# Kernel optimization log

Hardware: AMD Instinct MI355X
Metric: run time of the kernel (lower is better)

Reference implementation:

```python
import jax, jax.numpy as jnp
import numpy as np

# per-head local window sizes (== init local_region_shape); all divide H=W=64 -> no boundary masks
REGIONS = (4, 4, 8, 8, 16, 16, 32, 32)


def setup_inputs() -> dict:
    key = jax.random.key(0)
    ks = jax.random.split(key, 4)
    B, H, W, C = 4, 64, 64, 512
    N = H * W
    std = 0.02  # trunc_normal_(std=0.02) in the torch init
    return {
        "x": jax.random.normal(ks[0], (B, N, C), jnp.float32),
        "Wq": jax.random.normal(ks[1], (C, C), jnp.float32) * std,
        "Wkv": jax.random.normal(ks[2], (C, 2 * C), jnp.float32) * std,
        "Wproj": jax.random.normal(ks[3], (C, C), jnp.float32) * std,
        "bproj": jnp.zeros((C,), jnp.float32),
        "H": 64,
        "W": 64,
    }


def _to_windows(xh, H, W, r):
    # (B, N, d) -> (B*Hr*Wr, r*r, d), windows in row-major order (matches F.unfold k=stride=r)
    B, N, d = xh.shape
    Hr, Wr = H // r, W // r
    x = xh.reshape(B, Hr, r, Wr, r, d).transpose(0, 1, 3, 2, 4, 5)
    return x.reshape(B * Hr * Wr, r * r, d)


def _from_windows(xw, B, H, W, r):
    # inverse of _to_windows (matches F.fold k=stride=r)
    d = xw.shape[-1]
    Hr, Wr = H // r, W // r
    x = xw.reshape(B, Hr, Wr, r, r, d).transpose(0, 1, 3, 2, 4, 5)
    return x.reshape(B, H * W, d)


def reference(x, Wq, Wkv, Wproj, bproj, H, W):
    B, N, C = x.shape
    nh = len(REGIONS)
    hd = C // nh
    scale = hd ** -0.5
    q = (x @ Wq).reshape(B, N, nh, hd).transpose(0, 2, 1, 3)            # (B, nh, N, hd)
    kv = (x @ Wkv).reshape(B, N, 2, nh, hd).transpose(2, 0, 3, 1, 4)    # (2, B, nh, N, hd)
    k, v = kv[0], kv[1]
    outs = []
    for i, r in enumerate(REGIONS):
        qh, kh, vh = q[:, i], k[:, i], v[:, i]                          # (B, N, hd)
        if r == 1:
            attn = jax.nn.softmax(jnp.einsum("bqd,bkd->bqk", qh, kh) * scale, axis=-1)
            outs.append(jnp.einsum("bqk,bkd->bqd", attn, vh))
        else:
            qw = _to_windows(qh, H, W, r)                               # (B*nw, r*r, hd)
            kw = _to_windows(kh, H, W, r)
            vw = _to_windows(vh, H, W, r)
            attn = jax.nn.softmax(jnp.einsum("wqd,wkd->wqk", qw, kw) * scale, axis=-1)
            ow = jnp.einsum("wqk,wkd->wqd", attn, vw)
            outs.append(_from_windows(ow, B, H, W, r))
    o = jnp.stack(outs, axis=2).reshape(B, N, C)                        # heads interleaved per token
    return o @ Wproj + bproj
```

## Files before the change

kernel.cpp:

```cpp
#include <hip/hip_runtime.h>

typedef __attribute__((ext_vector_type(4))) float f32x4;
typedef __attribute__((ext_vector_type(8))) short s16x8;
typedef __attribute__((ext_vector_type(4))) unsigned int u32x4;
typedef __attribute__((ext_vector_type(2))) unsigned int u32x2;

#define LOG2E 1.44269504088896340736f

#define GLOAD_LDS16(g, l)                                                     \
    __builtin_amdgcn_global_load_lds((const __attribute__((address_space(1))) void*)(g), \
                                     (__attribute__((address_space(3))) void*)(l), 16, 0, 0)

__device__ inline unsigned short bf16_rne(float f) {
    unsigned u = __builtin_bit_cast(unsigned, f);
    unsigned r = u + 0x7FFFu + ((u >> 16) & 1u);
    return (unsigned short)(r >> 16);
}

__device__ inline f32x4 mfma16(s16x8 a, s16x8 b, f32x4 c) {
    return __builtin_amdgcn_mfma_f32_16x16x32_bf16(a, b, c, 0, 0, 0);
}


__global__ __launch_bounds__(256) void cvt_x_kernel(const float* __restrict__ x,
                                                    unsigned short* __restrict__ xb, int n8) {
    int i = blockIdx.x * 256 + threadIdx.x;
    if (i >= n8) return;
    const float4* xp = (const float4*)x + (size_t)i * 2;
    float4 a = xp[0], b = xp[1];
    unsigned short r[8] = {bf16_rne(a.x), bf16_rne(a.y), bf16_rne(a.z), bf16_rne(a.w),
                           bf16_rne(b.x), bf16_rne(b.y), bf16_rne(b.z), bf16_rne(b.w)};
    *(u32x4*)(xb + (size_t)i * 8) = *(u32x4*)r;
}

__global__ __launch_bounds__(256) void cvt_w_kernel(const float* __restrict__ Wq,
                                                    const float* __restrict__ Wkv,
                                                    const float* __restrict__ Wproj,
                                                    unsigned short* __restrict__ WcatT,
                                                    unsigned short* __restrict__ WprojT) {
    int i = blockIdx.x * 256 + threadIdx.x;
    if (i < 786432) {
        int n = i >> 9, k = i & 511;
        float v = (n < 512) ? Wq[k * 512 + n] : Wkv[k * 1024 + (n - 512)];
        WcatT[i] = bf16_rne(v);
    } else {
        int j = i - 786432;
        int n = j >> 9, k = j & 511;
        WprojT[j] = bf16_rne(Wproj[k * 512 + n]);
    }
}

__global__ __launch_bounds__(256) void vtrans_kernel(const unsigned short* __restrict__ vrow,
                                                     unsigned short* __restrict__ vT) {
    __shared__ unsigned short TT[64][72];
    int t = threadIdx.x;
    int t0 = (blockIdx.x & 255) * 64;
    int d0 = (blockIdx.x >> 8) * 64;
    int row = t >> 2, dseg = (t & 3) * 16;
    u32x4 a = *(const u32x4*)(vrow + (size_t)(t0 + row) * 512 + d0 + dseg);
    u32x4 b = *(const u32x4*)(vrow + (size_t)(t0 + row) * 512 + d0 + dseg + 8);
    *(u32x4*)&TT[row][dseg] = a;
    *(u32x4*)&TT[row][dseg + 8] = b;
    __syncthreads();
    int dim = t >> 2, tseg = (t & 3) * 16;
    unsigned short o[16];
#pragma unroll
    for (int j = 0; j < 16; j++) o[j] = TT[tseg + j][dim];
    *(u32x4*)(vT + (size_t)(d0 + dim) * 16384 + t0 + tseg) = *(u32x4*)o;
    *(u32x4*)(vT + (size_t)(d0 + dim) * 16384 + t0 + tseg + 8) = *((u32x4*)o + 1);
}


template <int MODE>
__global__ __launch_bounds__(256) void gemm128(const unsigned short* __restrict__ A,
                                               const unsigned short* __restrict__ BT,
                                               void* __restrict__ Cv,
                                               const float* __restrict__ bias,
                                               unsigned short* __restrict__ vrow,
                                               int M, int K, int ldc) {
    __shared__ unsigned short Alds[128 * 64];
    __shared__ unsigned short Blds[128 * 64];
    const int t = threadIdx.x, lane = t & 63;
    const int wv4 = t >> 6;
    const int wm = wv4 >> 1, wn = wv4 & 1;
    const int tm = blockIdx.y, tn = blockIdx.x;

    f32x4 acc[4][4];
#pragma unroll
    for (int mf = 0; mf < 4; mf++)
#pragma unroll
        for (int nf = 0; nf < 4; nf++) acc[mf][nf] = f32x4{0.f, 0.f, 0.f, 0.f};

    const int nkt = K >> 6;
    for (int kt = 0; kt < nkt; kt++) {
        __syncthreads();
#pragma unroll
        for (int i = 0; i < 4; i++) {
            int l = i * 256 + t;
            int row = l >> 3, u = l & 7;
            int us = u ^ (row & 7);
            GLOAD_LDS16(A + (size_t)(tm * 128 + row) * K + kt * 64 + us * 8,
                        (char*)Alds + l * 16);
            GLOAD_LDS16(BT + (size_t)(tn * 128 + row) * K + kt * 64 + us * 8,
                        (char*)Blds + l * 16);
        }
        __syncthreads();
#pragma unroll
        for (int ks = 0; ks < 2; ks++) {
            s16x8 af[4], bf[4];
#pragma unroll
            for (int mf = 0; mf < 4; mf++) {
                int row = wm * 64 + mf * 16 + (lane & 15);
                af[mf] = *(const s16x8*)((char*)Alds + row * 128 +
                                         ((((ks << 2) | (lane >> 4)) ^ (row & 7)) << 4));
            }
#pragma unroll
            for (int nf = 0; nf < 4; nf++) {
                int row = wn * 64 + nf * 16 + (lane & 15);
                bf[nf] = *(const s16x8*)((char*)Blds + row * 128 +
                                         ((((ks << 2) | (lane >> 4)) ^ (row & 7)) << 4));
            }
#pragma unroll
            for (int mf = 0; mf < 4; mf++)
#pragma unroll
                for (int nf = 0; nf < 4; nf++) acc[mf][nf] = mfma16(af[mf], bf[nf], acc[mf][nf]);
        }
    }

#pragma unroll
    for (int mf = 0; mf < 4; mf++) {
        int row0 = tm * 128 + wm * 64 + mf * 16 + (lane >> 4) * 4;
#pragma unroll
        for (int nf = 0; nf < 4; nf++) {
            int col = tn * 128 + wn * 64 + nf * 16 + (lane & 15);
            if constexpr (MODE == 1) {
                float bb = bias[col];
#pragma unroll
                for (int r = 0; r < 4; r++)
                    ((float*)Cv)[(size_t)(row0 + r) * ldc + col] = acc[mf][nf][r] + bb;
            } else {
                if (col < 1024) {
#pragma unroll
                    for (int r = 0; r < 4; r++)
                        ((unsigned short*)Cv)[(size_t)(row0 + r) * 1024 + col] =
                            bf16_rne(acc[mf][nf][r]);
                } else {
#pragma unroll
                    for (int r = 0; r < 4; r++)
                        vrow[(size_t)(row0 + r) * 512 + (col - 1024)] =
                            bf16_rne(acc[mf][nf][r]);
                }
            }
        }
    }
}


template <int R>
__device__ __forceinline__ void attn_body(int g, const unsigned short* __restrict__ qk,
                                          const unsigned short* __restrict__ vT,
                                          unsigned short* __restrict__ ob,
                                          char* smem, int lane, int wv) {
    constexpr int lR = (R == 8) ? 3 : ((R == 16) ? 4 : 5);
    constexpr int NCH = (R * R) / 64;
    constexpr int WPD = 64 / R;
    constexpr int NWIN = WPD * WPD;
    constexpr int HEAD0 = (R == 8) ? 2 : ((R == 16) ? 4 : 6);
    constexpr int BPW = (R * R) / 64;

    int wid = g / BPW, qc = g % BPW;
    int w = wid % NWIN, hb = wid / NWIN;
    int b = hb & 3, head = HEAD0 + (hb >> 2);
    int wy = w / WPD, wx = w % WPD;

    const int t = wv * 64 + lane;
    const int lc = lane & 15, lg = lane >> 4;
    const unsigned short* qbase = qk + (size_t)b * 4096 * 1024;
    const unsigned short* vbase = vT + (size_t)head * 64 * 16384 + b * 4096;
    const int wbase = wy * R * 64 + wx * R;

    char* Kb0 = smem;
    char* Vb0 = smem + 16384;
    unsigned short* pw = (unsigned short*)(smem + 32768) + wv * (16 * 64);

    int qrow = qc * 64 + wv * 16 + lc;
    int qn = wbase + (qrow >> lR) * 64 + (qrow & (R - 1));
    const unsigned short* qp = qbase + (size_t)qn * 1024 + head * 64 + lg * 8;
    s16x8 qf0 = *(const s16x8*)qp;
    s16x8 qf1 = *(const s16x8*)(qp + 32);

    f32x4 o[4];
    float mrun[4], lrun[4];
#pragma unroll
    for (int i = 0; i < 4; i++) {
        o[i] = f32x4{0.f, 0.f, 0.f, 0.f};
        mrun[i] = -1e30f;
        lrun[i] = 0.f;
    }

    auto stage = [&](int c, int buf) {
        char* Kd = Kb0 + buf * 8192;
        char* Vd = Vb0 + buf * 8192;
#pragma unroll
        for (int i = 0; i < 2; i++) {
            int l = i * 256 + t;
            int row = l >> 3, u = l & 7;
            {
                int us = u ^ (row & 7);
                int tok = c * 64 + row;
                int n = wbase + (tok >> lR) * 64 + (tok & (R - 1));
                GLOAD_LDS16(qbase + (size_t)n * 1024 + 512 + head * 64 + us * 8, Kd + l * 16);
            }
            {
                int us = u ^ (row & 7);
                int tok = c * 64 + us * 8;
                int n = wbase + (tok >> lR) * 64 + (tok & (R - 1));
                GLOAD_LDS16(vbase + (size_t)row * 16384 + n, Vd + l * 16);
            }
        }
    };

    stage(0, 0);
    int cur = 0;
    for (int c = 0; c < NCH; ++c) {
        if (c + 1 < NCH) {
            stage(c + 1, cur ^ 1);
            asm volatile("s_waitcnt vmcnt(4)" ::: "memory");
        } else {
            asm volatile("s_waitcnt vmcnt(0)" ::: "memory");
        }
        __builtin_amdgcn_sched_barrier(0);
        __builtin_amdgcn_s_barrier();
        char* Kd = Kb0 + cur * 8192;
        char* Vd = Vb0 + cur * 8192;

        f32x4 s[4];
#pragma unroll
        for (int cf = 0; cf < 4; cf++) s[cf] = f32x4{0.f, 0.f, 0.f, 0.f};
#pragma unroll
        for (int ks = 0; ks < 2; ks++) {
            s16x8 qf = ks ? qf1 : qf0;
#pragma unroll
            for (int cf = 0; cf < 4; cf++) {
                int tok = cf * 16 + lc;
                s16x8 kb = *(const s16x8*)(Kd + tok * 128 +
                                           ((((ks << 2) | lg) ^ (tok & 7)) << 4));
                s[cf] = mfma16(qf, kb, s[cf]);
            }
        }
#pragma unroll
        for (int cf = 0; cf < 4; cf++) s[cf] *= 0.125f;

        float pm[4];
#pragma unroll
        for (int r = 0; r < 4; r++)
            pm[r] = fmaxf(fmaxf(s[0][r], s[1][r]), fmaxf(s[2][r], s[3][r]));
#pragma unroll
        for (int m = 1; m < 16; m <<= 1)
#pragma unroll
            for (int r = 0; r < 4; r++) pm[r] = fmaxf(pm[r], __shfl_xor(pm[r], m, 64));

        float mnew[4], corr[4];
#pragma unroll
        for (int r = 0; r < 4; r++) {
            mnew[r] = fmaxf(mrun[r], pm[r]);
            corr[r] = exp2f((mrun[r] - mnew[r]) * LOG2E);
            mrun[r] = mnew[r];
        }
        float rs[4] = {0.f, 0.f, 0.f, 0.f};
        unsigned short pu[4][4];
#pragma unroll
        for (int cf = 0; cf < 4; cf++)
#pragma unroll
            for (int r = 0; r < 4; r++) {
                float p = exp2f((s[cf][r] - mnew[r]) * LOG2E);
                rs[r] += p;
                pu[cf][r] = bf16_rne(p);
            }
#pragma unroll
        for (int m = 1; m < 16; m <<= 1)
#pragma unroll
            for (int r = 0; r < 4; r++) rs[r] += __shfl_xor(rs[r], m, 64);
#pragma unroll
        for (int r = 0; r < 4; r++) lrun[r] = lrun[r] * corr[r] + rs[r];
#pragma unroll
        for (int nf = 0; nf < 4; nf++)
#pragma unroll
            for (int r = 0; r < 4; r++) o[nf][r] *= corr[r];

#pragma unroll
        for (int cf = 0; cf < 4; cf++) {
            int col = cf * 16 + lc;
#pragma unroll
            for (int r = 0; r < 4; r++) {
                int row = lg * 4 + r;
                *(unsigned short*)((char*)pw + row * 128 + (((col >> 3) ^ (row & 7)) << 4) +
                                   (col & 7) * 2) = pu[cf][r];
            }
        }
        asm volatile("s_waitcnt lgkmcnt(0)" ::: "memory");
        __builtin_amdgcn_sched_barrier(0);

#pragma unroll
        for (int ks = 0; ks < 2; ks++) {
            s16x8 pa = *(const s16x8*)((char*)pw + lc * 128 +
                                       ((((ks << 2) | lg) ^ (lc & 7)) << 4));
#pragma unroll
            for (int nf = 0; nf < 4; nf++) {
                int dim = nf * 16 + lc;
                s16x8 vb = *(const s16x8*)(Vd + dim * 128 +
                                           ((((ks << 2) | lg) ^ (dim & 7)) << 4));
                o[nf] = mfma16(pa, vb, o[nf]);
            }
        }
        __builtin_amdgcn_s_barrier();
        cur ^= 1;
    }

#pragma unroll
    for (int r = 0; r < 4; r++) {
        int qr = qc * 64 + wv * 16 + lg * 4 + r;
        int n = wbase + (qr >> lR) * 64 + (qr & (R - 1));
        float inv = 1.0f / lrun[r];
        unsigned short* op = ob + ((size_t)b * 4096 + n) * 512 + head * 64 + lc;
#pragma unroll
        for (int nf = 0; nf < 4; nf++) op[nf * 16] = bf16_rne(o[nf][r] * inv);
    }
}

__device__ __forceinline__ void attn4_body(int g, const unsigned short* __restrict__ qk,
                                           const unsigned short* __restrict__ vT,
                                           unsigned short* __restrict__ ob,
                                           char* smem, int lane, int wv) {
    unsigned short* vt = (unsigned short*)smem + wv * (64 * 32);
    unsigned short* pl = (unsigned short*)(smem + 16384) + wv * (16 * 32);
    const int lc = lane & 15, lg = lane >> 4;

    int gwin = g * 4 + wv;
    int w = gwin & 255, hb = gwin >> 8;
    int b = hb & 3, head = hb >> 2;
    int wy = w >> 4, wx = w & 15;
    const unsigned short* qbase = qk + (size_t)b * 4096 * 1024;

    int qn = (wy * 4 + (lc >> 2)) * 64 + wx * 4 + (lc & 3);
    const unsigned short* qp = qbase + (size_t)qn * 1024 + head * 64 + lg * 8;
    s16x8 qf0 = *(const s16x8*)qp;
    s16x8 qf1 = *(const s16x8*)(qp + 32);
    const unsigned short* kp = qbase + (size_t)qn * 1024 + 512 + head * 64 + lg * 8;
    s16x8 kb0 = *(const s16x8*)kp;
    s16x8 kb1 = *(const s16x8*)(kp + 32);

    f32x4 s = f32x4{0.f, 0.f, 0.f, 0.f};
    s = mfma16(qf0, kb0, s);
    s = mfma16(qf1, kb1, s);
    s *= 0.125f;

    {
        int d = lane;
        const unsigned short* vp = vT + (size_t)(head * 64 + d) * 16384 + b * 4096;
        char* vrowp = (char*)vt + d * 64;
#pragma unroll
        for (int tr = 0; tr < 4; tr++) {
            int n0 = (wy * 4 + tr) * 64 + wx * 4;
            u32x2 dv = *(const u32x2*)(vp + n0);
            *(u32x2*)(vrowp + (((tr >> 1) ^ (d & 3)) << 4) + (tr & 1) * 8) = dv;
        }
        u32x4 z = u32x4{0, 0, 0, 0};
        *(u32x4*)(vrowp + ((2 ^ (d & 3)) << 4)) = z;
        *(u32x4*)(vrowp + ((3 ^ (d & 3)) << 4)) = z;
    }

    float pm[4];
#pragma unroll
    for (int r = 0; r < 4; r++) pm[r] = s[r];
#pragma unroll
    for (int m = 1; m < 16; m <<= 1)
#pragma unroll
        for (int r = 0; r < 4; r++) pm[r] = fmaxf(pm[r], __shfl_xor(pm[r], m, 64));

    float l4[4];
    unsigned short pu[4];
#pragma unroll
    for (int r = 0; r < 4; r++) {
        float p = exp2f((s[r] - pm[r]) * LOG2E);
        pu[r] = bf16_rne(p);
        l4[r] = p;
    }
#pragma unroll
    for (int m = 1; m < 16; m <<= 1)
#pragma unroll
        for (int r = 0; r < 4; r++) l4[r] += __shfl_xor(l4[r], m, 64);

#pragma unroll
    for (int r = 0; r < 4; r++) {
        int row = lg * 4 + r;
        pl[row * 32 + lc] = pu[r];
        pl[row * 32 + 16 + lc] = 0;
    }
    asm volatile("s_waitcnt lgkmcnt(0)" ::: "memory");
    __builtin_amdgcn_sched_barrier(0);

    s16x8 pa = *(const s16x8*)(pl + lc * 32 + lg * 8);
    f32x4 o[4];
#pragma unroll
    for (int nf = 0; nf < 4; nf++) {
        int dim = nf * 16 + lc;
        s16x8 vb = *(const s16x8*)((char*)vt + dim * 64 + ((lg ^ (dim & 3)) << 4));
        o[nf] = mfma16(pa, vb, f32x4{0.f, 0.f, 0.f, 0.f});
    }

#pragma unroll
    for (int r = 0; r < 4; r++) {
        int qr = lg * 4 + r;
        int n = (wy * 4 + (qr >> 2)) * 64 + wx * 4 + (qr & 3);
        float inv = 1.0f / l4[r];
        unsigned short* op = ob + ((size_t)b * 4096 + n) * 512 + head * 64 + lc;
#pragma unroll
        for (int nf = 0; nf < 4; nf++) op[nf * 16] = bf16_rne(o[nf][r] * inv);
    }
}

__global__ __launch_bounds__(256) void attn_all(const unsigned short* __restrict__ qk,
                                                const unsigned short* __restrict__ vT,
                                                unsigned short* __restrict__ ob) {
    __shared__ __align__(16) char smem[40960];
    int t = threadIdx.x, lane = t & 63, wv = t >> 6;
    int g = blockIdx.x;
    if (g < 512) attn_body<32>(g, qk, vT, ob, smem, lane, wv);
    else if (g < 1024) attn_body<16>(g - 512, qk, vT, ob, smem, lane, wv);
    else if (g < 1536) attn_body<8>(g - 1024, qk, vT, ob, smem, lane, wv);
    else attn4_body(g - 1536, qk, vT, ob, smem, lane, wv);
}


extern "C" void kernel_launch(void* const* d_in, const int* in_sizes, int n_in,
                              void* d_out, int out_size, void* d_ws, size_t ws_size,
                              hipStream_t stream) {
    (void)in_sizes; (void)n_in; (void)out_size; (void)ws_size;
    const float* x = (const float*)d_in[0];
    const float* Wq = (const float*)d_in[1];
    const float* Wkv = (const float*)d_in[2];
    const float* Wproj = (const float*)d_in[3];
    const float* bproj = (const float*)d_in[4];

    char* ws = (char*)d_ws;
    unsigned short* qk = (unsigned short*)ws;
    unsigned short* vrow = (unsigned short*)(ws + (((size_t)32) << 20));
    unsigned short* xb = (unsigned short*)(ws + (((size_t)48) << 20));
    unsigned short* vT = xb;
    unsigned short* WcatT = (unsigned short*)(ws + (((size_t)64) << 20));
    unsigned short* WprojT = WcatT + (size_t)1536 * 512;
    unsigned short* ob = vrow;

    cvt_x_kernel<<<4096, 256, 0, stream>>>(x, xb, 16384 * 512 / 8);
    cvt_w_kernel<<<4096, 256, 0, stream>>>(Wq, Wkv, Wproj, WcatT, WprojT);

    gemm128<0><<<dim3(12, 128), 256, 0, stream>>>(xb, WcatT, (void*)qk, nullptr, vrow,
                                                  16384, 512, 1024);

    vtrans_kernel<<<2048, 256, 0, stream>>>(vrow, vT);

    attn_all<<<2048, 256, 0, stream>>>(qk, vT, ob);

    gemm128<1><<<dim3(4, 128), 256, 0, stream>>>(ob, WprojT, d_out, bproj, nullptr,
                                                 16384, 512, 512);
}
```

Measured before the change: 217.6 us.

## Process multiple query tiles per block to reuse staged K/V in windowed attention

The windowed attention body is templated on MT, so each block handles MT 16-row query tiles per wave against the same staged K/V chunks. This cuts repeated global-to-LDS K/V loads for the 32- and 16-wide windows, which now use MT=4 and shrink the grid from 2048 to 1280 blocks. It also raises wave priority (s_setprio) around the MFMA sections. The trade-off is fewer but much longer blocks for the large windows, which can hurt load balance and tail latency, plus higher register pressure from the per-tile accumulators.

```diff
diff --git a/kernel.cpp b/kernel.cpp
--- a/kernel.cpp
+++ b/kernel.cpp
@@ -156,19 +156,20 @@
 }
 
 
-template <int R>
-__device__ __forceinline__ void attn_body(int g, const unsigned short* __restrict__ qk,
-                                          const unsigned short* __restrict__ vT,
-                                          unsigned short* __restrict__ ob,
-                                          char* smem, int lane, int wv) {
+template <int R, int MT>
+__device__ __forceinline__ void attn_mt(int g, const unsigned short* __restrict__ qk,
+                                        const unsigned short* __restrict__ vT,
+                                        unsigned short* __restrict__ ob,
+                                        char* smem, int lane, int wv) {
     constexpr int lR = (R == 8) ? 3 : ((R == 16) ? 4 : 5);
-    constexpr int NCH = (R * R) / 64;
+    constexpr int L = R * R;
+    constexpr int NCH = L / 64;
     constexpr int WPD = 64 / R;
     constexpr int NWIN = WPD * WPD;
     constexpr int HEAD0 = (R == 8) ? 2 : ((R == 16) ? 4 : 6);
-    constexpr int BPW = (R * R) / 64;
-
-    int wid = g / BPW, qc = g % BPW;
+    constexpr int NWID = 4 * 2 * NWIN;
+
+    int wid = g % NWID, qc = g / NWID;
     int w = wid % NWIN, hb = wid / NWIN;
     int b = hb & 3, head = HEAD0 + (hb >> 2);
     int wy = w / WPD, wx = w % WPD;
@@ -183,20 +184,27 @@
     char* Vb0 = smem + 16384;
     unsigned short* pw = (unsigned short*)(smem + 32768) + wv * (16 * 64);
 
-    int qrow = qc * 64 + wv * 16 + lc;
-    int qn = wbase + (qrow >> lR) * 64 + (qrow & (R - 1));
-    const unsigned short* qp = qbase + (size_t)qn * 1024 + head * 64 + lg * 8;
-    s16x8 qf0 = *(const s16x8*)qp;
-    s16x8 qf1 = *(const s16x8*)(qp + 32);
-
-    f32x4 o[4];
-    float mrun[4], lrun[4];
-#pragma unroll
-    for (int i = 0; i < 4; i++) {
-        o[i] = f32x4{0.f, 0.f, 0.f, 0.f};
-        mrun[i] = -1e30f;
-        lrun[i] = 0.f;
-    }
+    const int qrow0 = qc * (MT * 64) + wv * (MT * 16);
+    s16x8 qf[MT][2];
+#pragma unroll
+    for (int m = 0; m < MT; m++) {
+        int qrow = qrow0 + m * 16 + lc;
+        int qn = wbase + (qrow >> lR) * 64 + (qrow & (R - 1));
+        const unsigned short* qp = qbase + (size_t)qn * 1024 + head * 64 + lg * 8;
+        qf[m][0] = *(const s16x8*)qp;
+        qf[m][1] = *(const s16x8*)(qp + 32);
+    }
+
+    f32x4 o[MT][4];
+    float mrun[MT][4], lrun[MT][4];
+#pragma unroll
+    for (int m = 0; m < MT; m++)
+#pragma unroll
+        for (int i = 0; i < 4; i++) {
+            o[m][i] = f32x4{0.f, 0.f, 0.f, 0.f};
+            mrun[m][i] = -1e30f;
+            lrun[m][i] = 0.f;
+        }
 
     auto stage = [&](int c, int buf) {
         char* Kd = Kb0 + buf * 8192;
@@ -205,14 +213,13 @@
         for (int i = 0; i < 2; i++) {
             int l = i * 256 + t;
             int row = l >> 3, u = l & 7;
+            int us = u ^ (row & 7);
             {
-                int us = u ^ (row & 7);
                 int tok = c * 64 + row;
                 int n = wbase + (tok >> lR) * 64 + (tok & (R - 1));
                 GLOAD_LDS16(qbase + (size_t)n * 1024 + 512 + head * 64 + us * 8, Kd + l * 16);
             }
             {
-                int us = u ^ (row & 7);
                 int tok = c * 64 + us * 8;
                 int n = wbase + (tok >> lR) * 64 + (tok & (R - 1));
                 GLOAD_LDS16(vbase + (size_t)row * 16384 + n, Vd + l * 16);
@@ -234,98 +241,106 @@
         char* Kd = Kb0 + cur * 8192;
         char* Vd = Vb0 + cur * 8192;
 
-        f32x4 s[4];
-#pragma unroll
-        for (int cf = 0; cf < 4; cf++) s[cf] = f32x4{0.f, 0.f, 0.f, 0.f};
-#pragma unroll
-        for (int ks = 0; ks < 2; ks++) {
-            s16x8 qf = ks ? qf1 : qf0;
+#pragma unroll
+        for (int m = 0; m < MT; m++) {
+            f32x4 s[4];
+#pragma unroll
+            for (int cf = 0; cf < 4; cf++) s[cf] = f32x4{0.f, 0.f, 0.f, 0.f};
+            __builtin_amdgcn_s_setprio(1);
+#pragma unroll
+            for (int ks = 0; ks < 2; ks++) {
+#pragma unroll
+                for (int cf = 0; cf < 4; cf++) {
+                    int tok = cf * 16 + lc;
+                    s16x8 kb = *(const s16x8*)(Kd + tok * 128 +
+                                               ((((ks << 2) | lg) ^ (tok & 7)) << 4));
+                    s[cf] = mfma16(qf[m][ks], kb, s[cf]);
+                }
+            }
+            __builtin_amdgcn_s_setprio(0);
+#pragma unroll
+            for (int cf = 0; cf < 4; cf++) s[cf] *= 0.125f;
+
+            float pm[4];
+#pragma unroll
+            for (int r = 0; r < 4; r++)
+                pm[r] = fmaxf(fmaxf(s[0][r], s[1][r]), fmaxf(s[2][r], s[3][r]));
+#pragma unroll
+            for (int mm = 1; mm < 16; mm <<= 1)
+#pragma unroll
+                for (int r = 0; r < 4; r++) pm[r] = fmaxf(pm[r], __shfl_xor(pm[r], mm, 64));
+
+            float mnew[4], corr[4];
+#pragma unroll
+            for (int r = 0; r < 4; r++) {
+                mnew[r] = fmaxf(mrun[m][r], pm[r]);
+                corr[r] = exp2f((mrun[m][r] - mnew[r]) * LOG2E);
+                mrun[m][r] = mnew[r];
+            }
+            float rs[4] = {0.f, 0.f, 0.f, 0.f};
+            unsigned short pu[4][4];
+#pragma unroll
+            for (int cf = 0; cf < 4; cf++)
+#pragma unroll
+                for (int r = 0; r < 4; r++) {
+                    float p = exp2f((s[cf][r] - mnew[r]) * LOG2E);
+                    rs[r] += p;
+                    pu[cf][r] = bf16_rne(p);
+                }
+#pragma unroll
+            for (int mm = 1; mm < 16; mm <<= 1)
+#pragma unroll
+                for (int r = 0; r < 4; r++) rs[r] += __shfl_xor(rs[r], mm, 64);
+#pragma unroll
+            for (int r = 0; r < 4; r++) lrun[m][r] = lrun[m][r] * corr[r] + rs[r];
+#pragma unroll
+            for (int nf = 0; nf < 4; nf++)
+#pragma unroll
+                for (int r = 0; r < 4; r++) o[m][nf][r] *= corr[r];
+
 #pragma unroll
             for (int cf = 0; cf < 4; cf++) {
-                int tok = cf * 16 + lc;
-                s16x8 kb = *(const s16x8*)(Kd + tok * 128 +
-                                           ((((ks << 2) | lg) ^ (tok & 7)) << 4));
-                s[cf] = mfma16(qf, kb, s[cf]);
-            }
-        }
-#pragma unroll
-        for (int cf = 0; cf < 4; cf++) s[cf] *= 0.125f;
-
-        float pm[4];
-#pragma unroll
-        for (int r = 0; r < 4; r++)
-            pm[r] = fmaxf(fmaxf(s[0][r], s[1][r]), fmaxf(s[2][r], s[3][r]));
-#pragma unroll
-        for (int m = 1; m < 16; m <<= 1)
-#pragma unroll
-            for (int r = 0; r < 4; r++) pm[r] = fmaxf(pm[r], __shfl_xor(pm[r], m, 64));
-
-        float mnew[4], corr[4];
-#pragma unroll
-        for (int r = 0; r < 4; r++) {
-            mnew[r] = fmaxf(mrun[r], pm[r]);
-            corr[r] = exp2f((mrun[r] - mnew[r]) * LOG2E);
-            mrun[r] = mnew[r];
-        }
-        float rs[4] = {0.f, 0.f, 0.f, 0.f};
-        unsigned short pu[4][4];
-#pragma unroll
-        for (int cf = 0; cf < 4; cf++)
-#pragma unroll
-            for (int r = 0; r < 4; r++) {
-                float p = exp2f((s[cf][r] - mnew[r]) * LOG2E);
-                rs[r] += p;
-                pu[cf][r] = bf16_rne(p);
-            }
-#pragma unroll
-        for (int m = 1; m < 16; m <<= 1)
-#pragma unroll
-            for (int r = 0; r < 4; r++) rs[r] += __shfl_xor(rs[r], m, 64);
-#pragma unroll
-        for (int r = 0; r < 4; r++) lrun[r] = lrun[r] * corr[r] + rs[r];
-#pragma unroll
-        for (int nf = 0; nf < 4; nf++)
-#pragma unroll
-            for (int r = 0; r < 4; r++) o[nf][r] *= corr[r];
-
-#pragma unroll
-        for (int cf = 0; cf < 4; cf++) {
-            int col = cf * 16 + lc;
-#pragma unroll
-            for (int r = 0; r < 4; r++) {
-                int row = lg * 4 + r;
-                *(unsigned short*)((char*)pw + row * 128 + (((col >> 3) ^ (row & 7)) << 4) +
-                                   (col & 7) * 2) = pu[cf][r];
-            }
-        }
-        asm volatile("s_waitcnt lgkmcnt(0)" ::: "memory");
-        __builtin_amdgcn_sched_barrier(0);
-
-#pragma unroll
-        for (int ks = 0; ks < 2; ks++) {
-            s16x8 pa = *(const s16x8*)((char*)pw + lc * 128 +
-                                       ((((ks << 2) | lg) ^ (lc & 7)) << 4));
-#pragma unroll
-            for (int nf = 0; nf < 4; nf++) {
-                int dim = nf * 16 + lc;
-                s16x8 vb = *(const s16x8*)(Vd + dim * 128 +
-                                           ((((ks << 2) | lg) ^ (dim & 7)) << 4));
-                o[nf] = mfma16(pa, vb, o[nf]);
-            }
+                int col = cf * 16 + lc;
+#pragma unroll
+                for (int r = 0; r < 4; r++) {
+                    int row = lg * 4 + r;
+                    *(unsigned short*)((char*)pw + row * 128 + (((col >> 3) ^ (row & 7)) << 4) +
+                                       (col & 7) * 2) = pu[cf][r];
+                }
+            }
+            asm volatile("s_waitcnt lgkmcnt(0)" ::: "memory");
+            __builtin_amdgcn_sched_barrier(0);
+
+            __builtin_amdgcn_s_setprio(1);
+#pragma unroll
+            for (int ks = 0; ks < 2; ks++) {
+                s16x8 pa = *(const s16x8*)((char*)pw + lc * 128 +
+                                           ((((ks << 2) | lg) ^ (lc & 7)) << 4));
+#pragma unroll
+                for (int nf = 0; nf < 4; nf++) {
+                    int dim = nf * 16 + lc;
+                    s16x8 vb = *(const s16x8*)(Vd + dim * 128 +
+                                               ((((ks << 2) | lg) ^ (dim & 7)) << 4));
+                    o[m][nf] = mfma16(pa, vb, o[m][nf]);
+                }
+            }
+            __builtin_amdgcn_s_setprio(0);
         }
         __builtin_amdgcn_s_barrier();
         cur ^= 1;
     }
 
 #pragma unroll
-    for (int r = 0; r < 4; r++) {
-        int qr = qc * 64 + wv * 16 + lg * 4 + r;
-        int n = wbase + (qr >> lR) * 64 + (qr & (R - 1));
-        float inv = 1.0f / lrun[r];
-        unsigned short* op = ob + ((size_t)b * 4096 + n) * 512 + head * 64 + lc;
-#pragma unroll
-        for (int nf = 0; nf < 4; nf++) op[nf * 16] = bf16_rne(o[nf][r] * inv);
-    }
+    for (int m = 0; m < MT; m++)
+#pragma unroll
+        for (int r = 0; r < 4; r++) {
+            int qr = qrow0 + m * 16 + lg * 4 + r;
+            int n = wbase + (qr >> lR) * 64 + (qr & (R - 1));
+            float inv = 1.0f / lrun[m][r];
+            unsigned short* op = ob + ((size_t)b * 4096 + n) * 512 + head * 64 + lc;
+#pragma unroll
+            for (int nf = 0; nf < 4; nf++) op[nf * 16] = bf16_rne(o[m][nf][r] * inv);
+        }
 }
 
 __device__ __forceinline__ void attn4_body(int g, const unsigned short* __restrict__ qk,
@@ -426,10 +441,10 @@
     __shared__ __align__(16) char smem[40960];
     int t = threadIdx.x, lane = t & 63, wv = t >> 6;
     int g = blockIdx.x;
-    if (g < 512) attn_body<32>(g, qk, vT, ob, smem, lane, wv);
-    else if (g < 1024) attn_body<16>(g - 512, qk, vT, ob, smem, lane, wv);
-    else if (g < 1536) attn_body<8>(g - 1024, qk, vT, ob, smem, lane, wv);
-    else attn4_body(g - 1536, qk, vT, ob, smem, lane, wv);
+    if (g < 128) attn_mt<32, 4>(g, qk, vT, ob, smem, lane, wv);
+    else if (g < 256) attn_mt<16, 4>(g - 128, qk, vT, ob, smem, lane, wv);
+    else if (g < 768) attn_mt<8, 1>(g - 256, qk, vT, ob, smem, lane, wv);
+    else attn4_body(g - 768, qk, vT, ob, smem, lane, wv);
 }
 
 
@@ -460,7 +475,7 @@
 
     vtrans_kernel<<<2048, 256, 0, stream>>>(vrow, vT);
 
-    attn_all<<<2048, 256, 0, stream>>>(qk, vT, ob);
+    attn_all<<<1280, 256, 0, stream>>>(qk, vT, ob);
 
     gemm128<1><<<dim3(4, 128), 256, 0, stream>>>(ob, WprojT, d_out, bproj, nullptr,
                                                  16384, 512, 512);
```

After: 262.7 us. 20.7% more time.
